# Kernel optimization log

Measured on AMD Instinct MI355X. Metric: run time of the kernel, lower is better.

Reference implementation:

```python
import jax, jax.numpy as jnp
import numpy as np

EMBED_DIM = 128
NUM_SYMBOLS = 200000
B = 1024
K = 200
PROCESS_STEPS = 4


def setup_inputs() -> dict:
    key = jax.random.key(0)
    ks = jax.random.split(key, 10)
    D = EMBED_DIM
    emb = jax.random.normal(ks[0], (NUM_SYMBOLS + 1, D), jnp.float32) * 0.02
    emb = emb.at[NUM_SYMBOLS].set(0.0)  # padding_idx row
    return {
        "relations": jax.random.randint(ks[1], (B, K), 0, NUM_SYMBOLS),
        "entities": jax.random.randint(ks[2], (B, K), 0, NUM_SYMBOLS),
        "query": jax.random.randint(ks[3], (B,), 0, NUM_SYMBOLS),
        "symbol_emb": emb,
        "gcn_w_w": jax.random.normal(ks[4], (D, 2 * D), jnp.float32) / np.sqrt(2 * D).astype(np.float32),
        "gcn_w_b": jnp.zeros((D,), jnp.float32),
        "p1_w": jax.random.normal(ks[5], (2 * D, D), jnp.float32) / np.sqrt(D).astype(np.float32),
        "p1_b": jnp.zeros((2 * D,), jnp.float32),
        "p2_w": jax.random.normal(ks[6], (D, 2 * D), jnp.float32) / np.sqrt(2 * D).astype(np.float32),
        "p2_b": jnp.zeros((D,), jnp.float32),
        "ln_a": jnp.ones((D,), jnp.float32),
        "ln_b": jnp.zeros((D,), jnp.float32),
        "w_ih": jax.random.normal(ks[7], (8 * D, D), jnp.float32) * 0.05,
        "w_hh": jax.random.normal(ks[8], (8 * D, 2 * D), jnp.float32) * 0.05,
        "b_ih": jnp.zeros((8 * D,), jnp.float32),
        "b_hh": jnp.zeros((8 * D,), jnp.float32),
    }


def _layer_norm(z, a, b, eps=1e-3):
    # repo's LayerNormalization: (z - mu) / (std + eps) * a + b, unbiased std
    mu = jnp.mean(z, axis=-1, keepdims=True)
    sigma = jnp.std(z, axis=-1, ddof=1, keepdims=True)
    return (z - mu) / (sigma + eps) * a + b


def _forward(symbol_emb, gcn_w_w, gcn_w_b, p1_w, p1_b, p2_w, p2_b,
             ln_a, ln_b, w_ih, w_hh, b_ih, b_hh,
             relations, entities, query):
    D = symbol_emb.shape[1]
    # --- neighbor_encoder: gather -> concat -> linear -> neighbor sum -> tanh
    rel_e = symbol_emb[relations]                       # (B, K, D)
    ent_e = symbol_emb[entities]                        # (B, K, D)
    concat = jnp.concatenate([rel_e, ent_e], axis=-1)   # (B, K, 2D)
    out = jnp.einsum('bkf,df->bkd', concat, gcn_w_w) + gcn_w_b
    num_neighbors = jnp.asarray(relations.shape[0], out.dtype)  # code uses relations.size()[0]
    support = jnp.tanh(out.sum(axis=1) / num_neighbors)  # (B, D)
    # --- SupportEncoder: FFN with residual + layernorm (dropout off in eval)
    hidden = jax.nn.relu(support @ p1_w.T + p1_b)        # (B, 2D)
    support_g = _layer_norm(hidden @ p2_w.T + p2_b + support, ln_a, ln_b)
    # --- QueryEncoder: LSTMCell(D, 2D) process block with attention over support
    q = symbol_emb[query]                                # (B, D)
    bsz = q.shape[0]
    h_r = jnp.zeros((bsz, 2 * D), q.dtype)
    c = jnp.zeros((bsz, 2 * D), q.dtype)
    h_out = q
    for _ in range(PROCESS_STEPS):
        gates = q @ w_ih.T + b_ih + h_r @ w_hh.T + b_hh  # (B, 8D)
        i, f, g, o = jnp.split(gates, 4, axis=-1)
        c = jax.nn.sigmoid(f) * c + jax.nn.sigmoid(i) * jnp.tanh(g)
        h_ = jax.nn.sigmoid(o) * jnp.tanh(c)             # (B, 2D)
        h_out = q + h_[:, :D]                            # (B, D)
        attn = jax.nn.softmax(h_out @ support_g.T, axis=1)  # (B, B)
        r = attn @ support_g                             # (B, D)
        h_r = jnp.concatenate([h_out, r], axis=-1)       # (B, 2D)
    query_embeds = h_out
    # --- cosine similarity over dim=1
    cross = jnp.sum(query_embeds * support_g, axis=1)
    n1 = jnp.sum(query_embeds * query_embeds, axis=1)
    n2 = jnp.sum(support_g * support_g, axis=1)
    return cross / jnp.sqrt(n1 * n2)                     # (B,)


def reference(relations, entities, query, symbol_emb, gcn_w_w, gcn_w_b,
              p1_w, p1_b, p2_w, p2_b, ln_a, ln_b, w_ih, w_hh, b_ih, b_hh):
    return _forward(symbol_emb, gcn_w_w, gcn_w_b, p1_w, p1_b, p2_w, p2_b,
                    ln_a, ln_b, w_ih, w_hh, b_ih, b_hh,
                    relations, entities, query)
```

## Files before the change

kernel.cpp:

```cpp
#include <hip/hip_runtime.h>
#include <math.h>

#define D 128
#define TWO_D 256
#define B_SZ 1024
#define KNB 200
#define AW 392
#define NKC 4

typedef _Float16 half8 __attribute__((ext_vector_type(8)));
typedef _Float16 half4 __attribute__((ext_vector_type(4)));
typedef float floatx4 __attribute__((ext_vector_type(4)));

__device__ __forceinline__ float sigmoid_f(float x) { return 1.f / (1.f + __expf(-x)); }
__device__ __forceinline__ float tanh_fast(float x) { return 1.f - 2.f / (__expf(2.f * x) + 1.f); }

__global__ __launch_bounds__(256) void k_cvtw(
    const float* __restrict__ w_ih, const float* __restrict__ w_hh,
    _Float16* __restrict__ w16)
{
    const int i8 = (blockIdx.x * 256 + threadIdx.x) * 8;
    const float* src = (i8 < 131072) ? (w_ih + i8) : (w_hh + (i8 - 131072));
    float4 v0 = *(const float4*)src;
    float4 v1 = *(const float4*)(src + 4);
    half8 h;
    h[0] = (_Float16)v0.x; h[1] = (_Float16)v0.y; h[2] = (_Float16)v0.z; h[3] = (_Float16)v0.w;
    h[4] = (_Float16)v1.x; h[5] = (_Float16)v1.y; h[6] = (_Float16)v1.z; h[7] = (_Float16)v1.w;
    *(half8*)&w16[i8] = h;
}

__global__ __launch_bounds__(512) void k_support(
    const int* __restrict__ relations, const int* __restrict__ entities,
    const int* __restrict__ query, const float* __restrict__ emb,
    const float* __restrict__ gcn_w, const float* __restrict__ gcn_b,
    const float* __restrict__ p1_w, const float* __restrict__ p1_b,
    const float* __restrict__ p2_w, const float* __restrict__ p2_b,
    const float* __restrict__ ln_a, const float* __restrict__ ln_b,
    float* __restrict__ sg, _Float16* __restrict__ sgH, _Float16* __restrict__ sgT,
    float* __restrict__ qbuf, _Float16* __restrict__ qbH)
{
    __shared__ int idxs[2 * KNB];
    __shared__ __align__(16) float part[16][132];
    __shared__ __align__(16) float S[TWO_D];
    __shared__ __align__(16) float sup[D];
    __shared__ __align__(16) float hid[TWO_D];
    __shared__ __align__(16) float zv[D];
    __shared__ float red2[2];

    const int b = blockIdx.x;
    const int t = threadIdx.x;

    if (t < KNB) idxs[t] = relations[b * KNB + t];
    else if (t < 2 * KNB) idxs[t] = entities[b * KNB + (t - KNB)];
    __syncthreads();

    {
        const int g = t >> 5, c4 = (t & 31) * 4;
        const int* mi = &idxs[(g >> 3) * KNB];
        float4 a4 = make_float4(0.f, 0.f, 0.f, 0.f);
        #pragma unroll 5
        for (int k = (g & 7); k < KNB; k += 8) {
            float4 v = *(const float4*)&emb[(size_t)mi[k] * D + c4];
            a4.x += v.x; a4.y += v.y; a4.z += v.z; a4.w += v.w;
        }
        *(float4*)&part[g][c4] = a4;
    }
    __syncthreads();
    if (t < TWO_D) {
        const int half = t >> 7, c = t & 127;
        float s = 0.f;
        #pragma unroll
        for (int j = 0; j < 8; ++j) s += part[half * 8 + j][c];
        S[t] = s;
    }
    __syncthreads();

    if (t < D) {
        const float4* w4 = (const float4*)(gcn_w + t * TWO_D);
        float dot = 0.f;
        #pragma unroll 8
        for (int f = 0; f < TWO_D / 4; ++f) {
            float4 w = w4[f];
            float4 s = *(const float4*)&S[f * 4];
            dot += w.x * s.x + w.y * s.y + w.z * s.z + w.w * s.w;
        }
        float v = (dot + 200.f * gcn_b[t]) * (1.f / 1024.f);
        sup[t] = tanhf(v);
    }
    __syncthreads();

    if (t < TWO_D) {
        const float4* w4 = (const float4*)(p1_w + t * D);
        float dot = 0.f;
        #pragma unroll 8
        for (int f = 0; f < D / 4; ++f) {
            float4 w = w4[f];
            float4 s = *(const float4*)&sup[f * 4];
            dot += w.x * s.x + w.y * s.y + w.z * s.z + w.w * s.w;
        }
        float h = dot + p1_b[t];
        hid[t] = h > 0.f ? h : 0.f;
    }
    __syncthreads();

    if (t < D) {
        const float4* w4 = (const float4*)(p2_w + t * TWO_D);
        float dot = 0.f;
        #pragma unroll 8
        for (int f = 0; f < TWO_D / 4; ++f) {
            float4 w = w4[f];
            float4 s = *(const float4*)&hid[f * 4];
            dot += w.x * s.x + w.y * s.y + w.z * s.z + w.w * s.w;
        }
        zv[t] = dot + p2_b[t] + sup[t];
    }
    __syncthreads();

    if (t < 64) {
        float x0 = zv[t], x1 = zv[t + 64];
        float s = x0 + x1;
        for (int off = 32; off; off >>= 1) s += __shfl_down(s, off);
        float mu = __shfl(s, 0) * (1.f / 128.f);
        float d0 = x0 - mu, d1 = x1 - mu;
        float v = d0 * d0 + d1 * d1;
        for (int off = 32; off; off >>= 1) v += __shfl_down(v, off);
        v = __shfl(v, 0);
        if (t == 0) { red2[0] = mu; red2[1] = sqrtf(v * (1.f / 127.f)); }
    }
    __syncthreads();
    if (t < D) {
        float mu = red2[0], sigma = red2[1];
        float val = (zv[t] - mu) / (sigma + 1e-3f) * ln_a[t] + ln_b[t];
        sg[b * D + t] = val;
        sgH[b * D + t] = (_Float16)val;
        sgT[t * B_SZ + b] = (_Float16)val;
        float qv = emb[(size_t)query[b] * D + t];
        qbuf[b * D + t] = qv;
        qbH[b * D + t] = (_Float16)qv;
    }
}

__global__ __launch_bounds__(256) void k_gates_mfma(
    const _Float16* __restrict__ qbH, const _Float16* __restrict__ hH,
    const float* __restrict__ rpart, const _Float16* __restrict__ w16,
    const float* __restrict__ b_ih, const float* __restrict__ b_hh,
    const float* __restrict__ qb,
    float* __restrict__ cbuf, float* __restrict__ hout,
    _Float16* __restrict__ houtH, int kend, int first)
{
    __shared__ _Float16 Ah[64 * AW];
    __shared__ _Float16 Bh[2][4][16][40];

    const int t = threadIdx.x;
    const int b0 = blockIdx.x * 64;
    const int n0 = blockIdx.y * 16;
    const int lane = t & 63, wv = t >> 6;
    const int m = lane & 15, quad = lane >> 4;

    {
        const int row = t >> 2;
        const int gr = b0 + row;
        for (int c4 = (t & 3) * 4; c4 < kend; c4 += 16) {
            half4 h;
            if (c4 < 128) {
                h = *(const half4*)&qbH[gr * D + c4];
            } else if (c4 < 256) {
                h = *(const half4*)&hH[gr * D + (c4 - 128)];
            } else {
                const int c = c4 - 256;
                float4 s4 = *(const float4*)&rpart[gr * D + c];
                #pragma unroll
                for (int j = 1; j < NKC; ++j) {
                    float4 v = *(const float4*)&rpart[j * (B_SZ * D) + gr * D + c];
                    s4.x += v.x; s4.y += v.y; s4.z += v.z; s4.w += v.w;
                }
                h[0] = (_Float16)s4.x; h[1] = (_Float16)s4.y;
                h[2] = (_Float16)s4.z; h[3] = (_Float16)s4.w;
            }
            *(half4*)&Ah[row * AW + c4] = h;
        }
    }

    const int sg_g = t >> 6, sg_u = (t >> 2) & 15, sg_kq = (t & 3) * 8;
    auto stage_b = [&](int ks, int buf) {
        const int grow = sg_g * 256 + n0 + sg_u;
        const int k0 = ks * 32 + sg_kq;
        const _Float16* src = (k0 < 128) ? &w16[grow * D + k0]
                                         : &w16[131072 + grow * TWO_D + (k0 - 128)];
        *(half8*)&Bh[buf][sg_g][sg_u][sg_kq] = *(const half8*)src;
    };

    stage_b(0, 0);
    __syncthreads();

    floatx4 acc[4];
    #pragma unroll
    for (int g = 0; g < 4; ++g)
        #pragma unroll
        for (int i = 0; i < 4; ++i) acc[g][i] = 0.f;

    const int nsteps = kend >> 5;
    for (int ks = 0; ks < nsteps; ++ks) {
        if (ks + 1 < nsteps) stage_b(ks + 1, (ks + 1) & 1);
        half8 a = *(const half8*)&Ah[(wv * 16 + m) * AW + ks * 32 + quad * 8];
        #pragma unroll
        for (int g = 0; g < 4; ++g) {
            half8 bf = *(const half8*)&Bh[ks & 1][g][m][quad * 8];
            acc[g] = __builtin_amdgcn_mfma_f32_16x16x32_f16(a, bf, acc[g], 0, 0, 0);
        }
        __syncthreads();
    }

    const int unit = n0 + m;
    float bi[4];
    #pragma unroll
    for (int g = 0; g < 4; ++g) bi[g] = b_ih[g * 256 + unit] + b_hh[g * 256 + unit];
    #pragma unroll
    for (int rr = 0; rr < 4; ++rr) {
        const int b = b0 + wv * 16 + quad * 4 + rr;
        float gi = acc[0][rr] + bi[0];
        float gf = acc[1][rr] + bi[1];
        float gg = acc[2][rr] + bi[2];
        float go = acc[3][rr] + bi[3];
        float cold = first ? 0.f : cbuf[b * TWO_D + unit];
        float cnew = sigmoid_f(gf) * cold + sigmoid_f(gi) * tanh_fast(gg);
        cbuf[b * TWO_D + unit] = cnew;
        if (n0 < D) {
            float h = sigmoid_f(go) * tanh_fast(cnew);
            float ho = qb[b * D + unit] + h;
            hout[b * D + unit] = ho;
            houtH[b * D + unit] = (_Float16)ho;
        }
    }
}

__global__ __launch_bounds__(256) void k_scores_mfma(
    const _Float16* __restrict__ hH, const _Float16* __restrict__ sgH,
    float* __restrict__ scores)
{
    const int t = threadIdx.x;
    const int lane = t & 63, wv = t >> 6;
    const int m = lane & 15, quad = lane >> 4;
    const int b0 = blockIdx.x * 64, j0 = blockIdx.y * 64;
    const int arow = b0 + wv * 16 + m;

    floatx4 acc[4];
    #pragma unroll
    for (int nt = 0; nt < 4; ++nt)
        #pragma unroll
        for (int i = 0; i < 4; ++i) acc[nt][i] = 0.f;

    #pragma unroll
    for (int ks = 0; ks < 4; ++ks) {
        const int k0 = ks * 32 + quad * 8;
        half8 a = *(const half8*)&hH[arow * D + k0];
        #pragma unroll
        for (int nt = 0; nt < 4; ++nt) {
            half8 bf = *(const half8*)&sgH[(j0 + nt * 16 + m) * D + k0];
            acc[nt] = __builtin_amdgcn_mfma_f32_16x16x32_f16(a, bf, acc[nt], 0, 0, 0);
        }
    }
    #pragma unroll
    for (int nt = 0; nt < 4; ++nt)
        #pragma unroll
        for (int rr = 0; rr < 4; ++rr)
            scores[(b0 + wv * 16 + quad * 4 + rr) * B_SZ + j0 + nt * 16 + m] = acc[nt][rr];
}

__global__ __launch_bounds__(256) void k_rgemm_mfma(
    const float* __restrict__ scores, const _Float16* __restrict__ sgT,
    float* __restrict__ rpart)
{
    __shared__ float st_lds[16][2];

    const int t = threadIdx.x;
    const int wv = t >> 6, lane = t & 63;
    const int m = lane & 15, quad = lane >> 4;
    const int m0 = blockIdx.x * 16;
    const int kbase = blockIdx.y * (B_SZ / NKC);

    #pragma unroll
    for (int r = 0; r < 4; ++r) {
        const int row = m0 + wv * 4 + r;
        const float* sp = &scores[row * B_SZ + lane * 16];
        float4 c0 = *(const float4*)sp;
        float4 c1 = *(const float4*)(sp + 4);
        float4 c2 = *(const float4*)(sp + 8);
        float4 c3 = *(const float4*)(sp + 12);
        float mm = fmaxf(fmaxf(fmaxf(c0.x, c0.y), fmaxf(c0.z, c0.w)),
                  fmaxf(fmaxf(fmaxf(c1.x, c1.y), fmaxf(c1.z, c1.w)),
                  fmaxf(fmaxf(fmaxf(c2.x, c2.y), fmaxf(c2.z, c2.w)),
                        fmaxf(fmaxf(c3.x, c3.y), fmaxf(c3.z, c3.w)))));
        for (int off = 32; off; off >>= 1) mm = fmaxf(mm, __shfl_down(mm, off));
        mm = __shfl(mm, 0);
        float ss = __expf(c0.x - mm) + __expf(c0.y - mm) + __expf(c0.z - mm) + __expf(c0.w - mm)
                 + __expf(c1.x - mm) + __expf(c1.y - mm) + __expf(c1.z - mm) + __expf(c1.w - mm)
                 + __expf(c2.x - mm) + __expf(c2.y - mm) + __expf(c2.z - mm) + __expf(c2.w - mm)
                 + __expf(c3.x - mm) + __expf(c3.y - mm) + __expf(c3.z - mm) + __expf(c3.w - mm);
        for (int off = 32; off; off >>= 1) ss += __shfl_down(ss, off);
        if (lane == 0) { st_lds[wv * 4 + r][0] = mm; st_lds[wv * 4 + r][1] = 1.f / ss; }
    }
    __syncthreads();
    const float stx = st_lds[m][0], sty = st_lds[m][1];

    floatx4 acc[2];
    #pragma unroll
    for (int nt = 0; nt < 2; ++nt)
        #pragma unroll
        for (int i = 0; i < 4; ++i) acc[nt][i] = 0.f;

    #pragma unroll
    for (int ks = 0; ks < (B_SZ / NKC) / 32; ++ks) {
        const int k0 = kbase + ks * 32 + quad * 8;
        const float* sp = &scores[(m0 + m) * B_SZ + k0];
        float4 v0 = *(const float4*)sp;
        float4 v1 = *(const float4*)(sp + 4);
        half8 a;
        a[0] = (_Float16)(__expf(v0.x - stx) * sty);
        a[1] = (_Float16)(__expf(v0.y - stx) * sty);
        a[2] = (_Float16)(__expf(v0.z - stx) * sty);
        a[3] = (_Float16)(__expf(v0.w - stx) * sty);
        a[4] = (_Float16)(__expf(v1.x - stx) * sty);
        a[5] = (_Float16)(__expf(v1.y - stx) * sty);
        a[6] = (_Float16)(__expf(v1.z - stx) * sty);
        a[7] = (_Float16)(__expf(v1.w - stx) * sty);
        #pragma unroll
        for (int nt = 0; nt < 2; ++nt) {
            const int col0 = (wv * 2 + nt) * 16;
            half8 bf = *(const half8*)&sgT[(col0 + m) * B_SZ + k0];
            acc[nt] = __builtin_amdgcn_mfma_f32_16x16x32_f16(a, bf, acc[nt], 0, 0, 0);
        }
    }
    float* rp = rpart + blockIdx.y * (B_SZ * D);
    #pragma unroll
    for (int nt = 0; nt < 2; ++nt)
        #pragma unroll
        for (int rr = 0; rr < 4; ++rr)
            rp[(m0 + quad * 4 + rr) * D + (wv * 2 + nt) * 16 + m] = acc[nt][rr];
}

__global__ __launch_bounds__(64) void k_cosine(
    const float* __restrict__ hout, const float* __restrict__ sg,
    float* __restrict__ out)
{
    const int b = blockIdx.x, t = threadIdx.x;
    float a0 = hout[b * D + t], a1 = hout[b * D + t + 64];
    float s0 = sg[b * D + t], s1 = sg[b * D + t + 64];
    float cr = a0 * s0 + a1 * s1;
    float n1 = a0 * a0 + a1 * a1;
    float n2 = s0 * s0 + s1 * s1;
    for (int off = 32; off; off >>= 1) {
        cr += __shfl_down(cr, off);
        n1 += __shfl_down(n1, off);
        n2 += __shfl_down(n2, off);
    }
    if (t == 0) out[b] = cr / sqrtf(n1 * n2);
}

extern "C" void kernel_launch(void* const* d_in, const int* in_sizes, int n_in,
                              void* d_out, int out_size, void* d_ws, size_t ws_size,
                              hipStream_t stream)
{
    const int*   relations = (const int*)d_in[0];
    const int*   entities  = (const int*)d_in[1];
    const int*   query     = (const int*)d_in[2];
    const float* emb       = (const float*)d_in[3];
    const float* gcn_w     = (const float*)d_in[4];
    const float* gcn_b     = (const float*)d_in[5];
    const float* p1_w      = (const float*)d_in[6];
    const float* p1_b      = (const float*)d_in[7];
    const float* p2_w      = (const float*)d_in[8];
    const float* p2_b      = (const float*)d_in[9];
    const float* ln_a      = (const float*)d_in[10];
    const float* ln_b      = (const float*)d_in[11];
    const float* w_ih      = (const float*)d_in[12];
    const float* w_hh      = (const float*)d_in[13];
    const float* b_ih      = (const float*)d_in[14];
    const float* b_hh      = (const float*)d_in[15];

    float* ws = (float*)d_ws;
    float*     sg     = ws;
    float*     qb     = ws + 131072;
    float*     hoA    = ws + 262144;
    float*     hoB    = ws + 393216;
    float*     cb     = ws + 524288;
    float*     scores = ws + 786432;
    float*     rpart  = ws + 1835008;
    _Float16*  sgH    = (_Float16*)(ws + 2359296);
    _Float16*  sgT    = (_Float16*)(ws + 2424832);
    _Float16*  qbH    = (_Float16*)(ws + 2490368);
    _Float16*  hHA    = (_Float16*)(ws + 2555904);
    _Float16*  hHB    = (_Float16*)(ws + 2621440);
    _Float16*  w16    = (_Float16*)(ws + 2686976);

    k_cvtw<<<dim3(192), dim3(256), 0, stream>>>(w_ih, w_hh, w16);
    k_support<<<dim3(B_SZ), dim3(512), 0, stream>>>(
        relations, entities, query, emb, gcn_w, gcn_b,
        p1_w, p1_b, p2_w, p2_b, ln_a, ln_b, sg, sgH, sgT, qb, qbH);

    k_gates_mfma<<<dim3(16, 16), dim3(256), 0, stream>>>(
        qbH, hHA, rpart, w16, b_ih, b_hh, qb, cb, hoB, hHB, 128, 1);
    k_scores_mfma<<<dim3(16, 16), dim3(256), 0, stream>>>(hHB, sgH, scores);
    k_rgemm_mfma<<<dim3(64, NKC), dim3(256), 0, stream>>>(scores, sgT, rpart);

    k_gates_mfma<<<dim3(16, 16), dim3(256), 0, stream>>>(
        qbH, hHB, rpart, w16, b_ih, b_hh, qb, cb, hoA, hHA, 384, 0);
    k_scores_mfma<<<dim3(16, 16), dim3(256), 0, stream>>>(hHA, sgH, scores);
    k_rgemm_mfma<<<dim3(64, NKC), dim3(256), 0, stream>>>(scores, sgT, rpart);

    k_gates_mfma<<<dim3(16, 16), dim3(256), 0, stream>>>(
        qbH, hHA, rpart, w16, b_ih, b_hh, qb, cb, hoB, hHB, 384, 0);
    k_scores_mfma<<<dim3(16, 16), dim3(256), 0, stream>>>(hHB, sgH, scores);
    k_rgemm_mfma<<<dim3(64, NKC), dim3(256), 0, stream>>>(scores, sgT, rpart);

    k_gates_mfma<<<dim3(16, 16), dim3(256), 0, stream>>>(
        qbH, hHB, rpart, w16, b_ih, b_hh, qb, cb, hoA, hHA, 384, 0);

    k_cosine<<<dim3(B_SZ), dim3(64), 0, stream>>>(hoA, sg, (float*)d_out);
}
```

Before: 319.2 us.

## Fuse LSTM process steps, attention and cosine into one persistent per-row-block kernel

Replaces the eleven per-step launches (gates, scores, softmax+rgemm, cosine) with a single kernel where each 512-thread block owns 16 query rows and runs all four process steps, keeping the cell state in registers and the scores, probabilities and hidden state in LDS. It also interleaves w_ih and w_hh into one row-major fp16 weight matrix and computes the query part of the gates once for reuse across steps. This removes launch overhead and the global round-trips for scores, rpart and cell state. In exchange it uses only 64 blocks, so much of the GPU sits idle, and each block rereads the full weights and support matrices from global memory.

```diff
diff --git a/kernel.cpp b/kernel.cpp
--- a/kernel.cpp
+++ b/kernel.cpp
@@ -2,11 +2,11 @@
 #include <math.h>
 
 #define D 128
-#define TWO_D 256
 #define B_SZ 1024
 #define KNB 200
 #define AW 392
-#define NKC 4
+#define SCW 1028
+#define PW 1032
 
 typedef _Float16 half8 __attribute__((ext_vector_type(8)));
 typedef _Float16 half4 __attribute__((ext_vector_type(4)));
@@ -20,7 +20,8 @@
     _Float16* __restrict__ w16)
 {
     const int i8 = (blockIdx.x * 256 + threadIdx.x) * 8;
-    const float* src = (i8 < 131072) ? (w_ih + i8) : (w_hh + (i8 - 131072));
+    const int row = i8 / 384, k = i8 % 384;
+    const float* src = (k < 128) ? &w_ih[row * 128 + k] : &w_hh[row * 256 + (k - 128)];
     float4 v0 = *(const float4*)src;
     float4 v1 = *(const float4*)(src + 4);
     half8 h;
@@ -37,13 +38,13 @@
     const float* __restrict__ p2_w, const float* __restrict__ p2_b,
     const float* __restrict__ ln_a, const float* __restrict__ ln_b,
     float* __restrict__ sg, _Float16* __restrict__ sgH, _Float16* __restrict__ sgT,
-    float* __restrict__ qbuf, _Float16* __restrict__ qbH)
+    _Float16* __restrict__ qbH)
 {
     __shared__ int idxs[2 * KNB];
     __shared__ __align__(16) float part[16][132];
-    __shared__ __align__(16) float S[TWO_D];
+    __shared__ __align__(16) float S[2 * D];
     __shared__ __align__(16) float sup[D];
-    __shared__ __align__(16) float hid[TWO_D];
+    __shared__ __align__(16) float hid[2 * D];
     __shared__ __align__(16) float zv[D];
     __shared__ float red2[2];
 
@@ -66,7 +67,7 @@
         *(float4*)&part[g][c4] = a4;
     }
     __syncthreads();
-    if (t < TWO_D) {
+    if (t < 2 * D) {
         const int half = t >> 7, c = t & 127;
         float s = 0.f;
         #pragma unroll
@@ -76,10 +77,10 @@
     __syncthreads();
 
     if (t < D) {
-        const float4* w4 = (const float4*)(gcn_w + t * TWO_D);
+        const float4* w4 = (const float4*)(gcn_w + t * 2 * D);
         float dot = 0.f;
         #pragma unroll 8
-        for (int f = 0; f < TWO_D / 4; ++f) {
+        for (int f = 0; f < 2 * D / 4; ++f) {
             float4 w = w4[f];
             float4 s = *(const float4*)&S[f * 4];
             dot += w.x * s.x + w.y * s.y + w.z * s.z + w.w * s.w;
@@ -89,7 +90,7 @@
     }
     __syncthreads();
 
-    if (t < TWO_D) {
+    if (t < 2 * D) {
         const float4* w4 = (const float4*)(p1_w + t * D);
         float dot = 0.f;
         #pragma unroll 8
@@ -104,10 +105,10 @@
     __syncthreads();
 
     if (t < D) {
-        const float4* w4 = (const float4*)(p2_w + t * TWO_D);
+        const float4* w4 = (const float4*)(p2_w + t * 2 * D);
         float dot = 0.f;
         #pragma unroll 8
-        for (int f = 0; f < TWO_D / 4; ++f) {
+        for (int f = 0; f < 2 * D / 4; ++f) {
             float4 w = w4[f];
             float4 s = *(const float4*)&hid[f * 4];
             dot += w.x * s.x + w.y * s.y + w.z * s.z + w.w * s.w;
@@ -134,227 +135,199 @@
         sg[b * D + t] = val;
         sgH[b * D + t] = (_Float16)val;
         sgT[t * B_SZ + b] = (_Float16)val;
-        float qv = emb[(size_t)query[b] * D + t];
-        qbuf[b * D + t] = qv;
-        qbH[b * D + t] = (_Float16)qv;
+        qbH[b * D + t] = (_Float16)emb[(size_t)query[b] * D + t];
     }
 }
 
-__global__ __launch_bounds__(256) void k_gates_mfma(
-    const _Float16* __restrict__ qbH, const _Float16* __restrict__ hH,
-    const float* __restrict__ rpart, const _Float16* __restrict__ w16,
-    const float* __restrict__ b_ih, const float* __restrict__ b_hh,
-    const float* __restrict__ qb,
-    float* __restrict__ cbuf, float* __restrict__ hout,
-    _Float16* __restrict__ houtH, int kend, int first)
+__global__ __launch_bounds__(512) void k_chain(
+    const _Float16* __restrict__ qbH, const _Float16* __restrict__ sgH,
+    const _Float16* __restrict__ sgT, const float* __restrict__ sg,
+    const _Float16* __restrict__ w16, const float* __restrict__ b_ih,
+    const float* __restrict__ b_hh, float* __restrict__ out)
 {
-    __shared__ _Float16 Ah[64 * AW];
-    __shared__ _Float16 Bh[2][4][16][40];
-
-    const int t = threadIdx.x;
-    const int b0 = blockIdx.x * 64;
-    const int n0 = blockIdx.y * 16;
-    const int lane = t & 63, wv = t >> 6;
-    const int m = lane & 15, quad = lane >> 4;
-
-    {
-        const int row = t >> 2;
-        const int gr = b0 + row;
-        for (int c4 = (t & 3) * 4; c4 < kend; c4 += 16) {
-            half4 h;
-            if (c4 < 128) {
-                h = *(const half4*)&qbH[gr * D + c4];
-            } else if (c4 < 256) {
-                h = *(const half4*)&hH[gr * D + (c4 - 128)];
-            } else {
-                const int c = c4 - 256;
-                float4 s4 = *(const float4*)&rpart[gr * D + c];
-                #pragma unroll
-                for (int j = 1; j < NKC; ++j) {
-                    float4 v = *(const float4*)&rpart[j * (B_SZ * D) + gr * D + c];
-                    s4.x += v.x; s4.y += v.y; s4.z += v.z; s4.w += v.w;
-                }
-                h[0] = (_Float16)s4.x; h[1] = (_Float16)s4.y;
-                h[2] = (_Float16)s4.z; h[3] = (_Float16)s4.w;
-            }
-            *(half4*)&Ah[row * AW + c4] = h;
-        }
-    }
-
-    const int sg_g = t >> 6, sg_u = (t >> 2) & 15, sg_kq = (t & 3) * 8;
-    auto stage_b = [&](int ks, int buf) {
-        const int grow = sg_g * 256 + n0 + sg_u;
-        const int k0 = ks * 32 + sg_kq;
-        const _Float16* src = (k0 < 128) ? &w16[grow * D + k0]
-                                         : &w16[131072 + grow * TWO_D + (k0 - 128)];
-        *(half8*)&Bh[buf][sg_g][sg_u][sg_kq] = *(const half8*)src;
-    };
-
-    stage_b(0, 0);
-    __syncthreads();
-
-    floatx4 acc[4];
-    #pragma unroll
-    for (int g = 0; g < 4; ++g)
-        #pragma unroll
-        for (int i = 0; i < 4; ++i) acc[g][i] = 0.f;
-
-    const int nsteps = kend >> 5;
-    for (int ks = 0; ks < nsteps; ++ks) {
-        if (ks + 1 < nsteps) stage_b(ks + 1, (ks + 1) & 1);
-        half8 a = *(const half8*)&Ah[(wv * 16 + m) * AW + ks * 32 + quad * 8];
-        #pragma unroll
-        for (int g = 0; g < 4; ++g) {
-            half8 bf = *(const half8*)&Bh[ks & 1][g][m][quad * 8];
-            acc[g] = __builtin_amdgcn_mfma_f32_16x16x32_f16(a, bf, acc[g], 0, 0, 0);
-        }
-        __syncthreads();
-    }
-
-    const int unit = n0 + m;
-    float bi[4];
-    #pragma unroll
-    for (int g = 0; g < 4; ++g) bi[g] = b_ih[g * 256 + unit] + b_hh[g * 256 + unit];
-    #pragma unroll
-    for (int rr = 0; rr < 4; ++rr) {
-        const int b = b0 + wv * 16 + quad * 4 + rr;
-        float gi = acc[0][rr] + bi[0];
-        float gf = acc[1][rr] + bi[1];
-        float gg = acc[2][rr] + bi[2];
-        float go = acc[3][rr] + bi[3];
-        float cold = first ? 0.f : cbuf[b * TWO_D + unit];
-        float cnew = sigmoid_f(gf) * cold + sigmoid_f(gi) * tanh_fast(gg);
-        cbuf[b * TWO_D + unit] = cnew;
-        if (n0 < D) {
-            float h = sigmoid_f(go) * tanh_fast(cnew);
-            float ho = qb[b * D + unit] + h;
-            hout[b * D + unit] = ho;
-            houtH[b * D + unit] = (_Float16)ho;
-        }
-    }
-}
-
-__global__ __launch_bounds__(256) void k_scores_mfma(
-    const _Float16* __restrict__ hH, const _Float16* __restrict__ sgH,
-    float* __restrict__ scores)
-{
-    const int t = threadIdx.x;
-    const int lane = t & 63, wv = t >> 6;
-    const int m = lane & 15, quad = lane >> 4;
-    const int b0 = blockIdx.x * 64, j0 = blockIdx.y * 64;
-    const int arow = b0 + wv * 16 + m;
-
-    floatx4 acc[4];
-    #pragma unroll
-    for (int nt = 0; nt < 4; ++nt)
-        #pragma unroll
-        for (int i = 0; i < 4; ++i) acc[nt][i] = 0.f;
-
-    #pragma unroll
-    for (int ks = 0; ks < 4; ++ks) {
-        const int k0 = ks * 32 + quad * 8;
-        half8 a = *(const half8*)&hH[arow * D + k0];
-        #pragma unroll
-        for (int nt = 0; nt < 4; ++nt) {
-            half8 bf = *(const half8*)&sgH[(j0 + nt * 16 + m) * D + k0];
-            acc[nt] = __builtin_amdgcn_mfma_f32_16x16x32_f16(a, bf, acc[nt], 0, 0, 0);
-        }
-    }
-    #pragma unroll
-    for (int nt = 0; nt < 4; ++nt)
-        #pragma unroll
-        for (int rr = 0; rr < 4; ++rr)
-            scores[(b0 + wv * 16 + quad * 4 + rr) * B_SZ + j0 + nt * 16 + m] = acc[nt][rr];
-}
-
-__global__ __launch_bounds__(256) void k_rgemm_mfma(
-    const float* __restrict__ scores, const _Float16* __restrict__ sgT,
-    float* __restrict__ rpart)
-{
-    __shared__ float st_lds[16][2];
+    __shared__ _Float16 Ah[16 * AW];
+    __shared__ float    Sc[16 * SCW];
+    __shared__ _Float16 P[16 * PW];
+    __shared__ float    smx[16];
+    __shared__ float    sinv[16];
+    __shared__ float    hsave[16 * 132];
 
     const int t = threadIdx.x;
     const int wv = t >> 6, lane = t & 63;
     const int m = lane & 15, quad = lane >> 4;
-    const int m0 = blockIdx.x * 16;
-    const int kbase = blockIdx.y * (B_SZ / NKC);
-
+    const int b0 = blockIdx.x * 16;
+
+    if (t < 256) {
+        const int row = t >> 4, ch = (t & 15) * 8;
+        *(half8*)&Ah[row * AW + ch] = *(const half8*)&qbH[(b0 + row) * D + ch];
+    }
+
+    float bi[2][4];
     #pragma unroll
-    for (int r = 0; r < 4; ++r) {
-        const int row = m0 + wv * 4 + r;
-        const float* sp = &scores[row * B_SZ + lane * 16];
-        float4 c0 = *(const float4*)sp;
-        float4 c1 = *(const float4*)(sp + 4);
-        float4 c2 = *(const float4*)(sp + 8);
-        float4 c3 = *(const float4*)(sp + 12);
-        float mm = fmaxf(fmaxf(fmaxf(c0.x, c0.y), fmaxf(c0.z, c0.w)),
-                  fmaxf(fmaxf(fmaxf(c1.x, c1.y), fmaxf(c1.z, c1.w)),
-                  fmaxf(fmaxf(fmaxf(c2.x, c2.y), fmaxf(c2.z, c2.w)),
-                        fmaxf(fmaxf(c3.x, c3.y), fmaxf(c3.z, c3.w)))));
-        for (int off = 32; off; off >>= 1) mm = fmaxf(mm, __shfl_down(mm, off));
-        mm = __shfl(mm, 0);
-        float ss = __expf(c0.x - mm) + __expf(c0.y - mm) + __expf(c0.z - mm) + __expf(c0.w - mm)
-                 + __expf(c1.x - mm) + __expf(c1.y - mm) + __expf(c1.z - mm) + __expf(c1.w - mm)
-                 + __expf(c2.x - mm) + __expf(c2.y - mm) + __expf(c2.z - mm) + __expf(c2.w - mm)
-                 + __expf(c3.x - mm) + __expf(c3.y - mm) + __expf(c3.z - mm) + __expf(c3.w - mm);
-        for (int off = 32; off; off >>= 1) ss += __shfl_down(ss, off);
-        if (lane == 0) { st_lds[wv * 4 + r][0] = mm; st_lds[wv * 4 + r][1] = 1.f / ss; }
-    }
-    __syncthreads();
-    const float stx = st_lds[m][0], sty = st_lds[m][1];
-
-    floatx4 acc[2];
+    for (int u = 0; u < 2; ++u) {
+        const int unit = wv * 32 + u * 16 + m;
+        #pragma unroll
+        for (int g = 0; g < 4; ++g) bi[u][g] = b_ih[g * 256 + unit] + b_hh[g * 256 + unit];
+    }
+
+    floatx4 cfr[2];
+    floatx4 gq[2][4];
+    floatx4 acc[2][4];
     #pragma unroll
-    for (int nt = 0; nt < 2; ++nt)
-        #pragma unroll
-        for (int i = 0; i < 4; ++i) acc[nt][i] = 0.f;
+    for (int u = 0; u < 2; ++u) {
+        #pragma unroll
+        for (int i = 0; i < 4; ++i) cfr[u][i] = 0.f;
+        #pragma unroll
+        for (int g = 0; g < 4; ++g)
+            #pragma unroll
+            for (int i = 0; i < 4; ++i) gq[u][g][i] = 0.f;
+    }
+
+    __syncthreads();
 
     #pragma unroll
-    for (int ks = 0; ks < (B_SZ / NKC) / 32; ++ks) {
-        const int k0 = kbase + ks * 32 + quad * 8;
-        const float* sp = &scores[(m0 + m) * B_SZ + k0];
-        float4 v0 = *(const float4*)sp;
-        float4 v1 = *(const float4*)(sp + 4);
-        half8 a;
-        a[0] = (_Float16)(__expf(v0.x - stx) * sty);
-        a[1] = (_Float16)(__expf(v0.y - stx) * sty);
-        a[2] = (_Float16)(__expf(v0.z - stx) * sty);
-        a[3] = (_Float16)(__expf(v0.w - stx) * sty);
-        a[4] = (_Float16)(__expf(v1.x - stx) * sty);
-        a[5] = (_Float16)(__expf(v1.y - stx) * sty);
-        a[6] = (_Float16)(__expf(v1.z - stx) * sty);
-        a[7] = (_Float16)(__expf(v1.w - stx) * sty);
-        #pragma unroll
-        for (int nt = 0; nt < 2; ++nt) {
-            const int col0 = (wv * 2 + nt) * 16;
-            half8 bf = *(const half8*)&sgT[(col0 + m) * B_SZ + k0];
-            acc[nt] = __builtin_amdgcn_mfma_f32_16x16x32_f16(a, bf, acc[nt], 0, 0, 0);
-        }
-    }
-    float* rp = rpart + blockIdx.y * (B_SZ * D);
+    for (int ks = 0; ks < 4; ++ks) {
+        half8 a = *(const half8*)&Ah[m * AW + ks * 32 + quad * 8];
+        #pragma unroll
+        for (int u = 0; u < 2; ++u)
+            #pragma unroll
+            for (int g = 0; g < 4; ++g) {
+                half8 bf = *(const half8*)&w16[(g * 256 + wv * 32 + u * 16 + m) * 384 + ks * 32 + quad * 8];
+                gq[u][g] = __builtin_amdgcn_mfma_f32_16x16x32_f16(a, bf, gq[u][g], 0, 0, 0);
+            }
+    }
+
+    auto gates_hr = [&]() {
+        #pragma unroll
+        for (int u = 0; u < 2; ++u)
+            #pragma unroll
+            for (int g = 0; g < 4; ++g) acc[u][g] = gq[u][g];
+        #pragma unroll
+        for (int ks = 0; ks < 8; ++ks) {
+            half8 a = *(const half8*)&Ah[m * AW + 128 + ks * 32 + quad * 8];
+            #pragma unroll
+            for (int u = 0; u < 2; ++u)
+                #pragma unroll
+                for (int g = 0; g < 4; ++g) {
+                    half8 bf = *(const half8*)&w16[(g * 256 + wv * 32 + u * 16 + m) * 384 + 128 + ks * 32 + quad * 8];
+                    acc[u][g] = __builtin_amdgcn_mfma_f32_16x16x32_f16(a, bf, acc[u][g], 0, 0, 0);
+                }
+        }
+    };
+
+    auto pointwise = [&](bool first, bool save) {
+        __syncthreads();
+        #pragma unroll
+        for (int u = 0; u < 2; ++u) {
+            const int unit = wv * 32 + u * 16 + m;
+            #pragma unroll
+            for (int rr = 0; rr < 4; ++rr) {
+                float gi = acc[u][0][rr] + bi[u][0];
+                float gf = acc[u][1][rr] + bi[u][1];
+                float gg = acc[u][2][rr] + bi[u][2];
+                float go = acc[u][3][rr] + bi[u][3];
+                float cold = first ? 0.f : cfr[u][rr];
+                float cn = sigmoid_f(gf) * cold + sigmoid_f(gi) * tanh_fast(gg);
+                cfr[u][rr] = cn;
+                if (wv < 4) {
+                    const int row = quad * 4 + rr;
+                    float qv = (float)Ah[row * AW + unit];
+                    float ho = qv + sigmoid_f(go) * tanh_fast(cn);
+                    Ah[row * AW + 128 + unit] = (_Float16)ho;
+                    if (save) hsave[row * 132 + unit] = ho;
+                }
+            }
+        }
+    };
+
+    auto attn = [&]() {
+        __syncthreads();
+        #pragma unroll
+        for (int i = 0; i < 8; ++i) {
+            const int j0 = (wv * 8 + i) * 16;
+            floatx4 a2;
+            #pragma unroll
+            for (int z = 0; z < 4; ++z) a2[z] = 0.f;
+            #pragma unroll
+            for (int ks = 0; ks < 4; ++ks) {
+                half8 a = *(const half8*)&Ah[m * AW + 128 + ks * 32 + quad * 8];
+                half8 bf = *(const half8*)&sgH[(j0 + m) * D + ks * 32 + quad * 8];
+                a2 = __builtin_amdgcn_mfma_f32_16x16x32_f16(a, bf, a2, 0, 0, 0);
+            }
+            #pragma unroll
+            for (int rr = 0; rr < 4; ++rr)
+                Sc[(quad * 4 + rr) * SCW + j0 + m] = a2[rr];
+        }
+        __syncthreads();
+        {
+            const int row = t >> 5, li = t & 31;
+            float mm = -1e30f;
+            #pragma unroll
+            for (int j = 0; j < 32; ++j) mm = fmaxf(mm, Sc[row * SCW + li + j * 32]);
+            #pragma unroll
+            for (int off = 16; off; off >>= 1) mm = fmaxf(mm, __shfl_down(mm, off));
+            if (li == 0) smx[row] = mm;
+        }
+        __syncthreads();
+        {
+            const int row = t >> 5, li = t & 31;
+            const float mm = smx[row];
+            float ss = 0.f;
+            #pragma unroll
+            for (int j = 0; j < 32; ++j) {
+                float e = __expf(Sc[row * SCW + li + j * 32] - mm);
+                P[row * PW + li + j * 32] = (_Float16)e;
+                ss += e;
+            }
+            #pragma unroll
+            for (int off = 16; off; off >>= 1) ss += __shfl_down(ss, off);
+            if (li == 0) sinv[row] = 1.f / ss;
+        }
+        __syncthreads();
+        {
+            floatx4 a3;
+            #pragma unroll
+            for (int z = 0; z < 4; ++z) a3[z] = 0.f;
+            #pragma unroll 8
+            for (int ks = 0; ks < 32; ++ks) {
+                half8 a = *(const half8*)&P[m * PW + ks * 32 + quad * 8];
+                half8 bf = *(const half8*)&sgT[(wv * 16 + m) * B_SZ + ks * 32 + quad * 8];
+                a3 = __builtin_amdgcn_mfma_f32_16x16x32_f16(a, bf, a3, 0, 0, 0);
+            }
+            #pragma unroll
+            for (int rr = 0; rr < 4; ++rr) {
+                const int row = quad * 4 + rr;
+                Ah[row * AW + 256 + wv * 16 + m] = (_Float16)(a3[rr] * sinv[row]);
+            }
+        }
+        __syncthreads();
+    };
+
     #pragma unroll
-    for (int nt = 0; nt < 2; ++nt)
-        #pragma unroll
-        for (int rr = 0; rr < 4; ++rr)
-            rp[(m0 + quad * 4 + rr) * D + (wv * 2 + nt) * 16 + m] = acc[nt][rr];
-}
-
-__global__ __launch_bounds__(64) void k_cosine(
-    const float* __restrict__ hout, const float* __restrict__ sg,
-    float* __restrict__ out)
-{
-    const int b = blockIdx.x, t = threadIdx.x;
-    float a0 = hout[b * D + t], a1 = hout[b * D + t + 64];
-    float s0 = sg[b * D + t], s1 = sg[b * D + t + 64];
-    float cr = a0 * s0 + a1 * s1;
-    float n1 = a0 * a0 + a1 * a1;
-    float n2 = s0 * s0 + s1 * s1;
-    for (int off = 32; off; off >>= 1) {
-        cr += __shfl_down(cr, off);
-        n1 += __shfl_down(n1, off);
-        n2 += __shfl_down(n2, off);
-    }
-    if (t == 0) out[b] = cr / sqrtf(n1 * n2);
+    for (int u = 0; u < 2; ++u)
+        #pragma unroll
+        for (int g = 0; g < 4; ++g) acc[u][g] = gq[u][g];
+    pointwise(true, false);
+    attn();
+    gates_hr(); pointwise(false, false); attn();
+    gates_hr(); pointwise(false, false); attn();
+    gates_hr(); pointwise(false, true);
+
+    __syncthreads();
+    if (t < 64) {
+        const int row = t & 15, part = t >> 4;
+        float cr = 0.f, n1 = 0.f, n2 = 0.f;
+        #pragma unroll 8
+        for (int j = 0; j < 32; ++j) {
+            const int c = part * 32 + j;
+            float h = hsave[row * 132 + c];
+            float s = sg[(b0 + row) * D + c];
+            cr += h * s; n1 += h * h; n2 += s * s;
+        }
+        cr += __shfl_down(cr, 16); n1 += __shfl_down(n1, 16); n2 += __shfl_down(n2, 16);
+        cr += __shfl_down(cr, 32); n1 += __shfl_down(n1, 32); n2 += __shfl_down(n2, 32);
+        if (t < 16) out[b0 + row] = cr / sqrtf(n1 * n2);
+    }
 }
 
 extern "C" void kernel_launch(void* const* d_in, const int* in_sizes, int n_in,
@@ -379,42 +352,16 @@
     const float* b_hh      = (const float*)d_in[15];
 
     float* ws = (float*)d_ws;
-    float*     sg     = ws;
-    float*     qb     = ws + 131072;
-    float*     hoA    = ws + 262144;
-    float*     hoB    = ws + 393216;
-    float*     cb     = ws + 524288;
-    float*     scores = ws + 786432;
-    float*     rpart  = ws + 1835008;
-    _Float16*  sgH    = (_Float16*)(ws + 2359296);
-    _Float16*  sgT    = (_Float16*)(ws + 2424832);
-    _Float16*  qbH    = (_Float16*)(ws + 2490368);
-    _Float16*  hHA    = (_Float16*)(ws + 2555904);
-    _Float16*  hHB    = (_Float16*)(ws + 2621440);
-    _Float16*  w16    = (_Float16*)(ws + 2686976);
+    float*     sg  = ws;
+    _Float16*  sgH = (_Float16*)(ws + 131072);
+    _Float16*  sgT = (_Float16*)(ws + 196608);
+    _Float16*  qbH = (_Float16*)(ws + 262144);
+    _Float16*  w16 = (_Float16*)(ws + 327680);
 
     k_cvtw<<<dim3(192), dim3(256), 0, stream>>>(w_ih, w_hh, w16);
     k_support<<<dim3(B_SZ), dim3(512), 0, stream>>>(
         relations, entities, query, emb, gcn_w, gcn_b,
-        p1_w, p1_b, p2_w, p2_b, ln_a, ln_b, sg, sgH, sgT, qb, qbH);
-
-    k_gates_mfma<<<dim3(16, 16), dim3(256), 0, stream>>>(
-        qbH, hHA, rpart, w16, b_ih, b_hh, qb, cb, hoB, hHB, 128, 1);
-    k_scores_mfma<<<dim3(16, 16), dim3(256), 0, stream>>>(hHB, sgH, scores);
-    k_rgemm_mfma<<<dim3(64, NKC), dim3(256), 0, stream>>>(scores, sgT, rpart);
-
-    k_gates_mfma<<<dim3(16, 16), dim3(256), 0, stream>>>(
-        qbH, hHB, rpart, w16, b_ih, b_hh, qb, cb, hoA, hHA, 384, 0);
-    k_scores_mfma<<<dim3(16, 16), dim3(256), 0, stream>>>(hHA, sgH, scores);
-    k_rgemm_mfma<<<dim3(64, NKC), dim3(256), 0, stream>>>(scores, sgT, rpart);
-
-    k_gates_mfma<<<dim3(16, 16), dim3(256), 0, stream>>>(
-        qbH, hHA, rpart, w16, b_ih, b_hh, qb, cb, hoB, hHB, 384, 0);
-    k_scores_mfma<<<dim3(16, 16), dim3(256), 0, stream>>>(hHB, sgH, scores);
-    k_rgemm_mfma<<<dim3(64, NKC), dim3(256), 0, stream>>>(scores, sgT, rpart);
-
-    k_gates_mfma<<<dim3(16, 16), dim3(256), 0, stream>>>(
-        qbH, hHB, rpart, w16, b_ih, b_hh, qb, cb, hoA, hHA, 384, 0);
-
-    k_cosine<<<dim3(B_SZ), dim3(64), 0, stream>>>(hoA, sg, (float*)d_out);
+        p1_w, p1_b, p2_w, p2_b, ln_a, ln_b, sg, sgH, sgT, qbH);
+    k_chain<<<dim3(64), dim3(512), 0, stream>>>(
+        qbH, sgH, sgT, sg, w16, b_ih, b_hh, (float*)d_out);
 }
```

Result: slower. 335.8 us (+5.2%).
